# Performance work log

Measured on AMD Instinct MI355X. Metric: run time of the kernel, lower is better.

## Reference

```python
import jax, jax.numpy as jnp
import numpy as np

N_NODES = 100000
N_EDGES = 1600000
IN_DIM, HIDDEN, OUT = 256, 128, 64


def setup_inputs() -> dict:
    key = jax.random.key(0)
    k1, k2, k3, k4 = jax.random.split(key, 4)
    x = jax.random.normal(k1, (N_NODES, IN_DIM), dtype=jnp.float32)
    edge_index = jax.random.randint(k2, (2, N_EDGES), 0, N_NODES, dtype=jnp.int32)
    # glorot-ish init for the GCN linear layers
    W1 = jax.random.normal(k3, (IN_DIM, HIDDEN), dtype=jnp.float32) / np.sqrt(IN_DIM)
    b1 = jnp.zeros((HIDDEN,), dtype=jnp.float32)
    W2 = jax.random.normal(k4, (HIDDEN, OUT), dtype=jnp.float32) / np.sqrt(HIDDEN)
    b2 = jnp.zeros((OUT,), dtype=jnp.float32)
    return {"x": x, "edge_index": edge_index, "W1": W1, "b1": b1, "W2": W2, "b2": b2}


def gcn_layer(x, src, dst, W, b):
    """PyG GCNConv: add self-loops, symmetric deg^-1/2 normalization,
    linear transform, scatter-add aggregation, bias."""
    h = x @ W  # [N, F_out]
    # degree over self-looped graph: in-degree(dst counts) + 1 self loop
    deg = jax.ops.segment_sum(jnp.ones((src.shape[0],), h.dtype), dst,
                              num_segments=N_NODES) + 1.0
    dinv = jax.lax.rsqrt(deg)  # [N]
    coef = dinv[src] * dinv[dst]  # [E]
    agg = jax.ops.segment_sum(h[src] * coef[:, None], dst, num_segments=N_NODES)
    # self-loop contribution (norm = dinv[i]^2) without materializing loop edges
    agg = agg + h * (dinv * dinv)[:, None]
    return agg + b


def reference(x, edge_index, W1, b1, W2, b2):
    src, dst = edge_index[0], edge_index[1]
    h = jax.nn.relu(gcn_layer(x, src, dst, W1, b1))
    return jax.nn.relu(gcn_layer(h, src, dst, W2, b2))
```

## Files before the change

### kernel.cpp

```cpp
#include <hip/hip_runtime.h>

#define N_NODES 100000
#define N_EDGES 1600000
#define IN_DIM 256
#define HIDDEN 128
#define OUT_DIM 64

#define NBIN 391
#define NBLK3 256
#define CHUNK 6250
#define NMAT (NBIN * NBLK3)
#define NBLK_SCAN (NMAT / 256)
#define CAP 6144

#define G1_TILES 782
#define G_HIST  160
#define G_SCAN1 120
#define G_SCAN2 60
#define G_SCAT  160
#define G_FINE  282
#define OFF_HIST  0
#define OFF_SCAN1 160
#define OFF_SCAN2 280
#define OFF_SCAT  340
#define OFF_FINE  500

#define CAPL1 640
#define CAPL2 1024

typedef __bf16 bf16x8 __attribute__((ext_vector_type(8)));
typedef __bf16 bf16x4 __attribute__((ext_vector_type(4)));
typedef float f32x4 __attribute__((ext_vector_type(4)));

__device__ __forceinline__ int bsw1h(int c, int kk) {
    return c * 128 + (kk ^ ((c & 7) << 3));
}

__device__ __forceinline__ void gemm1_tile(const float* __restrict__ X,
                                           const float* __restrict__ W1,
                                           __bf16* __restrict__ H,
                                           int bid, __bf16* Bs) {
    const int t = threadIdx.x;
    const int wave = t >> 6;
    const int lane = t & 63;
    const int lm = lane & 15;
    const int q = lane >> 4;
    const int row0 = bid * 128;
    const int g = row0 + wave * 16 + lm;

    f32x4 acc[8] = {};

    for (int half = 0; half < 2; ++half) {
        __syncthreads();
        for (int p = 0; p < 4; ++p) {
            int i = t + 512 * p;
            int c = i & 127;
            int kg = i >> 7;
            float v[8];
            #pragma unroll
            for (int j = 0; j < 8; ++j)
                v[j] = W1[(half * 128 + kg * 8 + j) * HIDDEN + c];
            bf16x8 w;
            #pragma unroll
            for (int j = 0; j < 8; ++j) w[j] = (__bf16)v[j];
            *(bf16x8*)&Bs[bsw1h(c, kg * 8)] = w;
        }
        __syncthreads();

        #pragma unroll
        for (int k0 = 0; k0 < 128; k0 += 32) {
            float4 v0 = make_float4(0.f, 0.f, 0.f, 0.f), v1 = v0;
            if (g < N_NODES) {
                const float* p = &X[(size_t)g * IN_DIM + half * 128 + k0 + q * 8];
                v0 = *(const float4*)p;
                v1 = *(const float4*)(p + 4);
            }
            bf16x8 a;
            a[0] = (__bf16)v0.x; a[1] = (__bf16)v0.y;
            a[2] = (__bf16)v0.z; a[3] = (__bf16)v0.w;
            a[4] = (__bf16)v1.x; a[5] = (__bf16)v1.y;
            a[6] = (__bf16)v1.z; a[7] = (__bf16)v1.w;
            #pragma unroll
            for (int ni = 0; ni < 8; ++ni) {
                bf16x8 bfr = *(const bf16x8*)&Bs[bsw1h(ni * 16 + lm, k0 + q * 8)];
                acc[ni] = __builtin_amdgcn_mfma_f32_16x16x32_bf16(a, bfr, acc[ni], 0, 0, 0);
            }
        }
    }

    #pragma unroll
    for (int r = 0; r < 4; ++r) {
        int grow = row0 + wave * 16 + q * 4 + r;
        if (grow < N_NODES) {
            #pragma unroll
            for (int ni = 0; ni < 8; ++ni)
                H[grow * HIDDEN + ni * 16 + lm] = (__bf16)acc[ni][r];
        }
    }
}

__global__ __launch_bounds__(512, 4)
void k_hist_g(const int* __restrict__ dst, int* __restrict__ cnt2,
              const float* __restrict__ X, const float* __restrict__ W1,
              __bf16* __restrict__ H) {
    __shared__ __attribute__((aligned(16))) char smem[32768];
    if (blockIdx.x < NBLK3) {
        int* hist = (int*)smem;
        int t = threadIdx.x;
        for (int i = t; i < NBIN; i += 512) hist[i] = 0;
        __syncthreads();
        int base = blockIdx.x * CHUNK;
        for (int i = t; i < CHUNK; i += 512)
            atomicAdd(&hist[dst[base + i] >> 8], 1);
        __syncthreads();
        for (int k = t; k < NBIN; k += 512)
            cnt2[k * NBLK3 + blockIdx.x] = hist[k];
    } else {
        gemm1_tile(X, W1, H, OFF_HIST + (int)blockIdx.x - NBLK3, (__bf16*)smem);
    }
}

__global__ __launch_bounds__(512, 4)
void k_scan1_g(int* __restrict__ a, int* __restrict__ bsum,
               const float* __restrict__ X, const float* __restrict__ W1,
               __bf16* __restrict__ H) {
    __shared__ __attribute__((aligned(16))) char smem[32768];
    if (blockIdx.x < NBLK_SCAN) {
        int* tmp = (int*)smem;
        int t = threadIdx.x;
        int i = blockIdx.x * 256 + t;
        int v = 0;
        if (t < 256) { v = a[i]; tmp[t] = v; }
        __syncthreads();
        #pragma unroll
        for (int off = 1; off < 256; off <<= 1) {
            int p = (t >= off && t < 256) ? tmp[t - off] : 0;
            __syncthreads();
            if (t < 256) tmp[t] += p;
            __syncthreads();
        }
        if (t < 256) a[i] = tmp[t] - v;
        if (t == 255) bsum[blockIdx.x] = tmp[255];
    } else {
        gemm1_tile(X, W1, H, OFF_SCAN1 + (int)blockIdx.x - NBLK_SCAN, (__bf16*)smem);
    }
}

__global__ __launch_bounds__(512, 4)
void k_scan2_g(int* __restrict__ bsum,
               const float* __restrict__ X, const float* __restrict__ W1,
               __bf16* __restrict__ H) {
    __shared__ __attribute__((aligned(16))) char smem[32768];
    if (blockIdx.x == 0) {
        int* tmp = (int*)smem;
        int t = threadIdx.x;
        int v = (t < NBLK_SCAN) ? bsum[t] : 0;
        tmp[t] = v;
        __syncthreads();
        #pragma unroll
        for (int off = 1; off < 512; off <<= 1) {
            int p = (t >= off) ? tmp[t - off] : 0;
            __syncthreads();
            tmp[t] += p;
            __syncthreads();
        }
        if (t < NBLK_SCAN) bsum[t] = tmp[t] - v;
    } else {
        gemm1_tile(X, W1, H, OFF_SCAN2 + (int)blockIdx.x - 1, (__bf16*)smem);
    }
}

__global__ __launch_bounds__(512, 4)
void k_scatter_g(const int* __restrict__ src, const int* __restrict__ dst,
                 const int* __restrict__ off2, const int* __restrict__ bsum,
                 unsigned int* __restrict__ ebuf,
                 const float* __restrict__ X, const float* __restrict__ W1,
                 __bf16* __restrict__ H) {
    __shared__ __attribute__((aligned(16))) char smem[32768];
    if (blockIdx.x < NBLK3) {
        int* cursor = (int*)smem;
        int t = threadIdx.x;
        for (int k = t; k < NBIN; k += 512)
            cursor[k] = off2[k * NBLK3 + blockIdx.x] + bsum[k];
        __syncthreads();
        int base = blockIdx.x * CHUNK;
        for (int i = t; i < CHUNK; i += 512) {
            int s = src[base + i], d = dst[base + i];
            int pos = atomicAdd(&cursor[d >> 8], 1);
            ebuf[pos] = ((unsigned)s << 8) | (unsigned)(d & 255);
        }
    } else {
        gemm1_tile(X, W1, H, OFF_SCAT + (int)blockIdx.x - NBLK3, (__bf16*)smem);
    }
}

struct FineSm {
    int hist[256];
    int tmp[256];
    int nodeoff[256];
    int cursor[256];
    unsigned int ed[CAP];
    int sOut[CAP];
};

__global__ __launch_bounds__(512, 4)
void k_fine_g(const unsigned int* __restrict__ ebuf, const int* __restrict__ off2,
              const int* __restrict__ bsum,
              int* __restrict__ esrc, int* __restrict__ rowstart,
              float* __restrict__ dinv,
              const float* __restrict__ X, const float* __restrict__ W1,
              __bf16* __restrict__ H) {
    __shared__ __attribute__((aligned(16))) char smem[sizeof(FineSm)];
    if (blockIdx.x < NBIN) {
        FineSm* sm = (FineSm*)smem;
        const int k = blockIdx.x;
        const int t = threadIdx.x;
        const int e0 = off2[k * NBLK3] + bsum[k];
        const int e1 = (k + 1 < NBIN) ? off2[(k + 1) * NBLK3] + bsum[k + 1] : N_EDGES;
        int m = e1 - e0;
        if (m > CAP) m = CAP;

        if (t < 256) sm->hist[t] = 0;
        __syncthreads();
        for (int i = t; i < m; i += 512) {
            unsigned v = ebuf[e0 + i];
            sm->ed[i] = v;
            atomicAdd(&sm->hist[v & 255], 1);
        }
        __syncthreads();

        int v = (t < 256) ? sm->hist[t] : 0;
        if (t < 256) sm->tmp[t] = v;
        __syncthreads();
        #pragma unroll
        for (int off = 1; off < 256; off <<= 1) {
            int p = (t >= off && t < 256) ? sm->tmp[t - off] : 0;
            __syncthreads();
            if (t < 256) sm->tmp[t] += p;
            __syncthreads();
        }
        if (t < 256) {
            sm->nodeoff[t] = sm->tmp[t] - v;
            sm->cursor[t] = sm->tmp[t] - v;
        }
        __syncthreads();

        for (int i = t; i < m; i += 512) {
            unsigned e = sm->ed[i];
            int pos = atomicAdd(&sm->cursor[e & 255], 1);
            sm->sOut[pos] = (int)(e >> 8);
        }
        __syncthreads();

        for (int i = t; i < m; i += 512) esrc[e0 + i] = sm->sOut[i];

        if (t < 256) {
            int n = k * 256 + t;
            if (n < N_NODES) {
                rowstart[n] = e0 + sm->nodeoff[t];
                dinv[n] = rsqrtf((float)sm->hist[t] + 1.0f);
            }
        }
        if (k == 0 && t == 0) rowstart[N_NODES] = N_EDGES;
    } else {
        gemm1_tile(X, W1, H, OFF_FINE + (int)blockIdx.x - NBIN, (__bf16*)smem);
    }
}

__launch_bounds__(256)
__global__ void k_gather1(const int* __restrict__ rowstart, const int* __restrict__ esrc,
                          const float* __restrict__ dinv,
                          const __bf16* __restrict__ H, const float* __restrict__ b1,
                          __bf16* __restrict__ AGG) {
    __shared__ int eidx[CAPL1];
    const int nb = blockIdx.x * 16;
    const int t = threadIdx.x;
    const int e0 = rowstart[nb];
    const int m = rowstart[nb + 16] - e0;
    for (int i = t; i < m && i < CAPL1; i += 256) eidx[i] = esrc[e0 + i];
    __syncthreads();

    const int n = nb + (t >> 4);
    const int j = (t & 15) * 8;

    float dn = dinv[n];
    float s = dn * dn;
    bf16x8 h = *(const bf16x8*)&H[n * HIDDEN + j];
    float acc[8];
    #pragma unroll
    for (int i = 0; i < 8; ++i) acc[i] = (float)h[i] * s;

    int p = rowstart[n] - e0, p1 = rowstart[n + 1] - e0;
    if (p1 <= CAPL1) {
        for (; p + 3 < p1; p += 4) {
            int s0 = eidx[p + 0], s1 = eidx[p + 1], s2 = eidx[p + 2], s3 = eidx[p + 3];
            float c0 = dinv[s0] * dn, c1 = dinv[s1] * dn;
            float c2 = dinv[s2] * dn, c3 = dinv[s3] * dn;
            bf16x8 v0 = *(const bf16x8*)&H[s0 * HIDDEN + j];
            bf16x8 v1 = *(const bf16x8*)&H[s1 * HIDDEN + j];
            bf16x8 v2 = *(const bf16x8*)&H[s2 * HIDDEN + j];
            bf16x8 v3 = *(const bf16x8*)&H[s3 * HIDDEN + j];
            #pragma unroll
            for (int i = 0; i < 8; ++i) acc[i] = fmaf((float)v0[i], c0, acc[i]);
            #pragma unroll
            for (int i = 0; i < 8; ++i) acc[i] = fmaf((float)v1[i], c1, acc[i]);
            #pragma unroll
            for (int i = 0; i < 8; ++i) acc[i] = fmaf((float)v2[i], c2, acc[i]);
            #pragma unroll
            for (int i = 0; i < 8; ++i) acc[i] = fmaf((float)v3[i], c3, acc[i]);
        }
        for (; p < p1; ++p) {
            int sidx = eidx[p];
            float c = dinv[sidx] * dn;
            bf16x8 v = *(const bf16x8*)&H[sidx * HIDDEN + j];
            #pragma unroll
            for (int i = 0; i < 8; ++i) acc[i] = fmaf((float)v[i], c, acc[i]);
        }
    } else {
        const int* ep = esrc + e0;
        for (; p + 3 < p1; p += 4) {
            int s0 = ep[p + 0], s1 = ep[p + 1], s2 = ep[p + 2], s3 = ep[p + 3];
            float c0 = dinv[s0] * dn, c1 = dinv[s1] * dn;
            float c2 = dinv[s2] * dn, c3 = dinv[s3] * dn;
            bf16x8 v0 = *(const bf16x8*)&H[s0 * HIDDEN + j];
            bf16x8 v1 = *(const bf16x8*)&H[s1 * HIDDEN + j];
            bf16x8 v2 = *(const bf16x8*)&H[s2 * HIDDEN + j];
            bf16x8 v3 = *(const bf16x8*)&H[s3 * HIDDEN + j];
            #pragma unroll
            for (int i = 0; i < 8; ++i) acc[i] = fmaf((float)v0[i], c0, acc[i]);
            #pragma unroll
            for (int i = 0; i < 8; ++i) acc[i] = fmaf((float)v1[i], c1, acc[i]);
            #pragma unroll
            for (int i = 0; i < 8; ++i) acc[i] = fmaf((float)v2[i], c2, acc[i]);
            #pragma unroll
            for (int i = 0; i < 8; ++i) acc[i] = fmaf((float)v3[i], c3, acc[i]);
        }
        for (; p < p1; ++p) {
            int sidx = ep[p];
            float c = dinv[sidx] * dn;
            bf16x8 v = *(const bf16x8*)&H[sidx * HIDDEN + j];
            #pragma unroll
            for (int i = 0; i < 8; ++i) acc[i] = fmaf((float)v[i], c, acc[i]);
        }
    }

    float4 bb0 = *(const float4*)&b1[j];
    float4 bb1 = *(const float4*)&b1[j + 4];
    bf16x8 o;
    o[0] = (__bf16)fmaxf(acc[0] + bb0.x, 0.f);
    o[1] = (__bf16)fmaxf(acc[1] + bb0.y, 0.f);
    o[2] = (__bf16)fmaxf(acc[2] + bb0.z, 0.f);
    o[3] = (__bf16)fmaxf(acc[3] + bb0.w, 0.f);
    o[4] = (__bf16)fmaxf(acc[4] + bb1.x, 0.f);
    o[5] = (__bf16)fmaxf(acc[5] + bb1.y, 0.f);
    o[6] = (__bf16)fmaxf(acc[6] + bb1.z, 0.f);
    o[7] = (__bf16)fmaxf(acc[7] + bb1.w, 0.f);
    *(bf16x8*)&AGG[n * HIDDEN + j] = o;
}

__device__ __forceinline__ int bsw2(int c, int kk) {
    return c * 128 + (kk ^ ((c & 7) << 3));
}

__launch_bounds__(512, 8)
__global__ void k_gemm2(const __bf16* __restrict__ AGG, const float* __restrict__ W2,
                        __bf16* __restrict__ H2) {
    __shared__ __attribute__((aligned(16))) __bf16 Bs[64 * 128];

    const int t = threadIdx.x;
    const int wave = t >> 6;
    const int lane = t & 63;
    const int lm = lane & 15;
    const int q = lane >> 4;
    const int row0 = blockIdx.x * 128;
    const int g = row0 + wave * 16 + lm;

    for (int p = 0; p < 2; ++p) {
        int i = t + 512 * p;
        int c = i & 63;
        int kg = i >> 6;
        float v[8];
        #pragma unroll
        for (int j = 0; j < 8; ++j)
            v[j] = W2[(kg * 8 + j) * OUT_DIM + c];
        bf16x8 w;
        #pragma unroll
        for (int j = 0; j < 8; ++j) w[j] = (__bf16)v[j];
        *(bf16x8*)&Bs[bsw2(c, kg * 8)] = w;
    }
    __syncthreads();

    f32x4 acc[4] = {};

    #pragma unroll
    for (int k0 = 0; k0 < HIDDEN; k0 += 32) {
        bf16x8 a = {};
        if (g < N_NODES)
            a = *(const bf16x8*)&AGG[(size_t)g * HIDDEN + k0 + q * 8];
        #pragma unroll
        for (int ni = 0; ni < 4; ++ni) {
            bf16x8 bfr = *(const bf16x8*)&Bs[bsw2(ni * 16 + lm, k0 + q * 8)];
            acc[ni] = __builtin_amdgcn_mfma_f32_16x16x32_bf16(a, bfr, acc[ni], 0, 0, 0);
        }
    }

    #pragma unroll
    for (int r = 0; r < 4; ++r) {
        int grow = row0 + wave * 16 + q * 4 + r;
        if (grow < N_NODES) {
            #pragma unroll
            for (int ni = 0; ni < 4; ++ni)
                H2[grow * OUT_DIM + ni * 16 + lm] = (__bf16)acc[ni][r];
        }
    }
}

__launch_bounds__(256)
__global__ void k_gather2(const int* __restrict__ rowstart, const int* __restrict__ esrc,
                          const float* __restrict__ dinv,
                          const __bf16* __restrict__ H2, const float* __restrict__ b2,
                          float* __restrict__ OUT) {
    __shared__ int eidx[CAPL2];
    const int nb = blockIdx.x * 32;
    const int t = threadIdx.x;
    const int e0 = rowstart[nb];
    const int m = rowstart[nb + 32] - e0;
    for (int i = t; i < m && i < CAPL2; i += 256) eidx[i] = esrc[e0 + i];
    __syncthreads();

    const int n = nb + (t >> 3);
    const int j = (t & 7) * 8;

    float dn = dinv[n];
    float s = dn * dn;
    bf16x8 h = *(const bf16x8*)&H2[n * OUT_DIM + j];
    float acc[8];
    #pragma unroll
    for (int i = 0; i < 8; ++i) acc[i] = (float)h[i] * s;

    int p = rowstart[n] - e0, p1 = rowstart[n + 1] - e0;
    if (p1 <= CAPL2) {
        for (; p + 3 < p1; p += 4) {
            int s0 = eidx[p + 0], s1 = eidx[p + 1], s2 = eidx[p + 2], s3 = eidx[p + 3];
            float c0 = dinv[s0] * dn, c1 = dinv[s1] * dn;
            float c2 = dinv[s2] * dn, c3 = dinv[s3] * dn;
            bf16x8 v0 = *(const bf16x8*)&H2[s0 * OUT_DIM + j];
            bf16x8 v1 = *(const bf16x8*)&H2[s1 * OUT_DIM + j];
            bf16x8 v2 = *(const bf16x8*)&H2[s2 * OUT_DIM + j];
            bf16x8 v3 = *(const bf16x8*)&H2[s3 * OUT_DIM + j];
            #pragma unroll
            for (int i = 0; i < 8; ++i) acc[i] = fmaf((float)v0[i], c0, acc[i]);
            #pragma unroll
            for (int i = 0; i < 8; ++i) acc[i] = fmaf((float)v1[i], c1, acc[i]);
            #pragma unroll
            for (int i = 0; i < 8; ++i) acc[i] = fmaf((float)v2[i], c2, acc[i]);
            #pragma unroll
            for (int i = 0; i < 8; ++i) acc[i] = fmaf((float)v3[i], c3, acc[i]);
        }
        for (; p < p1; ++p) {
            int sidx = eidx[p];
            float c = dinv[sidx] * dn;
            bf16x8 v = *(const bf16x8*)&H2[sidx * OUT_DIM + j];
            #pragma unroll
            for (int i = 0; i < 8; ++i) acc[i] = fmaf((float)v[i], c, acc[i]);
        }
    } else {
        const int* ep = esrc + e0;
        for (; p + 3 < p1; p += 4) {
            int s0 = ep[p + 0], s1 = ep[p + 1], s2 = ep[p + 2], s3 = ep[p + 3];
            float c0 = dinv[s0] * dn, c1 = dinv[s1] * dn;
            float c2 = dinv[s2] * dn, c3 = dinv[s3] * dn;
            bf16x8 v0 = *(const bf16x8*)&H2[s0 * OUT_DIM + j];
            bf16x8 v1 = *(const bf16x8*)&H2[s1 * OUT_DIM + j];
            bf16x8 v2 = *(const bf16x8*)&H2[s2 * OUT_DIM + j];
            bf16x8 v3 = *(const bf16x8*)&H2[s3 * OUT_DIM + j];
            #pragma unroll
            for (int i = 0; i < 8; ++i) acc[i] = fmaf((float)v0[i], c0, acc[i]);
            #pragma unroll
            for (int i = 0; i < 8; ++i) acc[i] = fmaf((float)v1[i], c1, acc[i]);
            #pragma unroll
            for (int i = 0; i < 8; ++i) acc[i] = fmaf((float)v2[i], c2, acc[i]);
            #pragma unroll
            for (int i = 0; i < 8; ++i) acc[i] = fmaf((float)v3[i], c3, acc[i]);
        }
        for (; p < p1; ++p) {
            int sidx = ep[p];
            float c = dinv[sidx] * dn;
            bf16x8 v = *(const bf16x8*)&H2[sidx * OUT_DIM + j];
            #pragma unroll
            for (int i = 0; i < 8; ++i) acc[i] = fmaf((float)v[i], c, acc[i]);
        }
    }

    float4 bb0 = *(const float4*)&b2[j];
    float4 bb1 = *(const float4*)&b2[j + 4];
    float4 o0, o1;
    o0.x = fmaxf(acc[0] + bb0.x, 0.f);
    o0.y = fmaxf(acc[1] + bb0.y, 0.f);
    o0.z = fmaxf(acc[2] + bb0.z, 0.f);
    o0.w = fmaxf(acc[3] + bb0.w, 0.f);
    o1.x = fmaxf(acc[4] + bb1.x, 0.f);
    o1.y = fmaxf(acc[5] + bb1.y, 0.f);
    o1.z = fmaxf(acc[6] + bb1.z, 0.f);
    o1.w = fmaxf(acc[7] + bb1.w, 0.f);
    *(float4*)&OUT[n * OUT_DIM + j] = o0;
    *(float4*)&OUT[n * OUT_DIM + j + 4] = o1;
}

extern "C" void kernel_launch(void* const* d_in, const int* in_sizes, int n_in,
                              void* d_out, int out_size, void* d_ws, size_t ws_size,
                              hipStream_t stream) {
    const float* x  = (const float*)d_in[0];
    const int* ei   = (const int*)d_in[1];
    const float* W1 = (const float*)d_in[2];
    const float* b1 = (const float*)d_in[3];
    const float* W2 = (const float*)d_in[4];
    const float* b2 = (const float*)d_in[5];
    float* out = (float*)d_out;

    const int* src = ei;
    const int* dst = ei + N_EDGES;

    char* ws = (char*)d_ws;
    int*          cnt2     = (int*)         (ws + 0x000000);
    int*          bsum     = (int*)         (ws + 0x080000);
    int*          rowstart = (int*)         (ws + 0x090000);
    float*        dinv     = (float*)       (ws + 0x100000);
    unsigned int* ebuf     = (unsigned int*)(ws + 0x180000);
    int*          esrc     = (int*)         (ws + 0x800000);
    __bf16*       h1       = (__bf16*)      (ws + 0xE80000);
    __bf16*       agg1     = (__bf16*)      (ws + 0x2880000);
    __bf16*       h2       = (__bf16*)      (ws + 0x4280000);

    k_hist_g   <<<NBLK3     + G_HIST,  512, 0, stream>>>(dst, cnt2, x, W1, h1);
    k_scan1_g  <<<NBLK_SCAN + G_SCAN1, 512, 0, stream>>>(cnt2, bsum, x, W1, h1);
    k_scan2_g  <<<1         + G_SCAN2, 512, 0, stream>>>(bsum, x, W1, h1);
    k_scatter_g<<<NBLK3     + G_SCAT,  512, 0, stream>>>(src, dst, cnt2, bsum, ebuf,
                                                         x, W1, h1);
    k_fine_g   <<<NBIN      + G_FINE,  512, 0, stream>>>(ebuf, cnt2, bsum, esrc,
                                                         rowstart, dinv, x, W1, h1);

    k_gather1<<<N_NODES / 16, 256, 0, stream>>>(rowstart, esrc, dinv, h1, b1, agg1);
    k_gemm2<<<(N_NODES + 127) / 128, 512, 0, stream>>>(agg1, W2, h2);
    k_gather2<<<N_NODES / 32, 256, 0, stream>>>(rowstart, esrc, dinv, h2, b2, out);
}
```

Before: 329.5 us.

## Fuse layer-2 GEMM into layer-1 gather kernel via LDS tile

The layer-1 aggregation kernel now writes each block's 16 aggregated rows into a swizzled LDS tile and immediately multiplies it by W2 with MFMA, producing H2 directly. This removes the separate k_gemm2 launch and the round trip of the 100000x128 bf16 intermediate through global memory. In exchange, every one of the 6250 gather blocks reloads and converts the full 128x64 W2 into LDS and adds an extra barrier, and the larger LDS footprint may reduce occupancy of the latency-bound gather.

After: 320.7 us. 2.7% less time.

```diff
diff --git a/kernel.cpp b/kernel.cpp
--- a/kernel.cpp
+++ b/kernel.cpp
@@ -267,21 +267,46 @@
     }
 }
 
+__device__ __forceinline__ int bsw2(int c, int kk) {
+    return c * 128 + (kk ^ ((c & 7) << 3));
+}
+
 __launch_bounds__(256)
-__global__ void k_gather1(const int* __restrict__ rowstart, const int* __restrict__ esrc,
-                          const float* __restrict__ dinv,
-                          const __bf16* __restrict__ H, const float* __restrict__ b1,
-                          __bf16* __restrict__ AGG) {
+__global__ void k_gather1f(const int* __restrict__ rowstart, const int* __restrict__ esrc,
+                           const float* __restrict__ dinv,
+                           const __bf16* __restrict__ H, const float* __restrict__ b1,
+                           const float* __restrict__ W2,
+                           __bf16* __restrict__ H2) {
     __shared__ int eidx[CAPL1];
+    __shared__ __attribute__((aligned(16))) __bf16 As[16 * 128];
+    __shared__ __attribute__((aligned(16))) __bf16 Bs[64 * 128];
+
+    const int t = threadIdx.x;
     const int nb = blockIdx.x * 16;
-    const int t = threadIdx.x;
     const int e0 = rowstart[nb];
     const int m = rowstart[nb + 16] - e0;
+
+    #pragma unroll
+    for (int p = 0; p < 4; ++p) {
+        int i = t + 256 * p;
+        int c = i & 63;
+        int kg = i >> 6;
+        float v[8];
+        #pragma unroll
+        for (int jj = 0; jj < 8; ++jj)
+            v[jj] = W2[(kg * 8 + jj) * OUT_DIM + c];
+        bf16x8 w;
+        #pragma unroll
+        for (int jj = 0; jj < 8; ++jj) w[jj] = (__bf16)v[jj];
+        *(bf16x8*)&Bs[bsw2(c, kg * 8)] = w;
+    }
     for (int i = t; i < m && i < CAPL1; i += 256) eidx[i] = esrc[e0 + i];
     __syncthreads();
 
-    const int n = nb + (t >> 4);
-    const int j = (t & 15) * 8;
+    const int nl = t >> 4;
+    const int n = nb + nl;
+    const int jc = t & 15;
+    const int j = jc * 8;
 
     float dn = dinv[n];
     float s = dn * dn;
@@ -355,64 +380,25 @@
     o[5] = (__bf16)fmaxf(acc[5] + bb1.y, 0.f);
     o[6] = (__bf16)fmaxf(acc[6] + bb1.z, 0.f);
     o[7] = (__bf16)fmaxf(acc[7] + bb1.w, 0.f);
-    *(bf16x8*)&AGG[n * HIDDEN + j] = o;
-}
-
-__device__ __forceinline__ int bsw2(int c, int kk) {
-    return c * 128 + (kk ^ ((c & 7) << 3));
-}
-
-__launch_bounds__(512, 8)
-__global__ void k_gemm2(const __bf16* __restrict__ AGG, const float* __restrict__ W2,
-                        __bf16* __restrict__ H2) {
-    __shared__ __attribute__((aligned(16))) __bf16 Bs[64 * 128];
-
-    const int t = threadIdx.x;
+    *(bf16x8*)&As[nl * 128 + (jc ^ (nl & 7)) * 8] = o;
+    __syncthreads();
+
     const int wave = t >> 6;
     const int lane = t & 63;
     const int lm = lane & 15;
     const int q = lane >> 4;
-    const int row0 = blockIdx.x * 128;
-    const int g = row0 + wave * 16 + lm;
-
-    for (int p = 0; p < 2; ++p) {
-        int i = t + 512 * p;
-        int c = i & 63;
-        int kg = i >> 6;
-        float v[8];
-        #pragma unroll
-        for (int j = 0; j < 8; ++j)
-            v[j] = W2[(kg * 8 + j) * OUT_DIM + c];
-        bf16x8 w;
-        #pragma unroll
-        for (int j = 0; j < 8; ++j) w[j] = (__bf16)v[j];
-        *(bf16x8*)&Bs[bsw2(c, kg * 8)] = w;
-    }
-    __syncthreads();
-
-    f32x4 acc[4] = {};
-
+
+    f32x4 acc2 = {};
     #pragma unroll
     for (int k0 = 0; k0 < HIDDEN; k0 += 32) {
-        bf16x8 a = {};
-        if (g < N_NODES)
-            a = *(const bf16x8*)&AGG[(size_t)g * HIDDEN + k0 + q * 8];
-        #pragma unroll
-        for (int ni = 0; ni < 4; ++ni) {
-            bf16x8 bfr = *(const bf16x8*)&Bs[bsw2(ni * 16 + lm, k0 + q * 8)];
-            acc[ni] = __builtin_amdgcn_mfma_f32_16x16x32_bf16(a, bfr, acc[ni], 0, 0, 0);
-        }
-    }
-
+        int c = (k0 >> 3) + q;
+        bf16x8 a = *(const bf16x8*)&As[lm * 128 + (c ^ (lm & 7)) * 8];
+        bf16x8 bfr = *(const bf16x8*)&Bs[bsw2(wave * 16 + lm, k0 + q * 8)];
+        acc2 = __builtin_amdgcn_mfma_f32_16x16x32_bf16(a, bfr, acc2, 0, 0, 0);
+    }
     #pragma unroll
-    for (int r = 0; r < 4; ++r) {
-        int grow = row0 + wave * 16 + q * 4 + r;
-        if (grow < N_NODES) {
-            #pragma unroll
-            for (int ni = 0; ni < 4; ++ni)
-                H2[grow * OUT_DIM + ni * 16 + lm] = (__bf16)acc[ni][r];
-        }
-    }
+    for (int r = 0; r < 4; ++r)
+        H2[(nb + q * 4 + r) * OUT_DIM + wave * 16 + lm] = (__bf16)acc2[r];
 }
 
 __launch_bounds__(256)
@@ -529,7 +515,6 @@
     unsigned int* ebuf     = (unsigned int*)(ws + 0x180000);
     int*          esrc     = (int*)         (ws + 0x800000);
     __bf16*       h1       = (__bf16*)      (ws + 0xE80000);
-    __bf16*       agg1     = (__bf16*)      (ws + 0x2880000);
     __bf16*       h2       = (__bf16*)      (ws + 0x4280000);
 
     k_hist_g   <<<NBLK3     + G_HIST,  512, 0, stream>>>(dst, cnt2, x, W1, h1);
@@ -540,7 +525,6 @@
     k_fine_g   <<<NBIN      + G_FINE,  512, 0, stream>>>(ebuf, cnt2, bsum, esrc,
                                                          rowstart, dinv, x, W1, h1);
 
-    k_gather1<<<N_NODES / 16, 256, 0, stream>>>(rowstart, esrc, dinv, h1, b1, agg1);
-    k_gemm2<<<(N_NODES + 127) / 128, 512, 0, stream>>>(agg1, W2, h2);
+    k_gather1f<<<N_NODES / 16, 256, 0, stream>>>(rowstart, esrc, dinv, h1, b1, W2, h2);
     k_gather2<<<N_NODES / 32, 256, 0, stream>>>(rowstart, esrc, dinv, h2, b2, out);
 }
```
